# Kernel optimization log

Measured on AMD Instinct MI355X. Metric: run time of the kernel, lower is better.

The kernel has to match this reference:

```python
import jax, jax.numpy as jnp
import numpy as np

BETA = 0.6666666666666666
ZETA = 1.1
GAMMA = -0.1

B, N, D = 256, 128, 64


def setup_inputs() -> dict:
    key = jax.random.key(0)
    kq, kk, kv, km = jax.random.split(key, 4)
    query = jax.random.normal(kq, (B, 1, N, 1, D), dtype=jnp.float32)
    key_t = jax.random.normal(kk, (B, 1, N, 1, D), dtype=jnp.float32)
    value = jax.random.normal(kv, (B, 1, N, 1, D), dtype=jnp.float32)
    # nn.Parameter init: normal(mean=0, std=0.001)
    matrix = jax.random.normal(km, (N, N, D, D), dtype=jnp.float32) * 0.001
    return {"query": query, "key": key_t, "value": value, "matrix": matrix}


def _hard_concrete_gate(log_alpha):
    # deterministic (eval-mode) hard-concrete gate
    s = jax.nn.sigmoid(log_alpha) * (ZETA - GAMMA) + GAMMA
    z = jnp.clip(s, 0.0, 1.0)
    # expected L0 penalty
    l0 = jnp.sum(jax.nn.sigmoid(log_alpha - BETA * np.log(-GAMMA / ZETA)))
    return z, l0


def reference(query, key, value, matrix):
    d = query.shape[-1]
    q = query[:, 0, :, 0, :]   # [B, N, D]
    k = key[:, 0, :, 0, :]     # [B, N, D]
    v = value[:, 0, :, 0, :]   # [B, N, D]
    z, l0 = _hard_concrete_gate(matrix)  # z: [N, N, D, D]
    # score[b,i,j] = sum_{d,e} q[b,i,d] * k[b,j,e] * z[i,j,d,e] / sqrt(D)
    # fused bilinear contraction (no (B,N,N,D,D) intermediate)
    score = jnp.einsum('bid,ijde,bje->bij', q, z, k) / jnp.asarray(
        float(d) ** 0.5, q.dtype)
    attn = jax.nn.softmax(score, axis=-1)          # [B, N, N]
    out = jnp.einsum('bij,bjd->bid', attn, v)      # [B, N, D]
    return out, l0
```

## Files before the change

### kernel.cpp

```cpp
#include <hip/hip_runtime.h>
#include <hip/hip_bf16.h>

#define B_ 256
#define N_ 128
#define D_ 64

typedef short bf16x8 __attribute__((ext_vector_type(8)));
typedef short bf16x4 __attribute__((ext_vector_type(4)));
typedef float f32x4 __attribute__((ext_vector_type(4)));

static __device__ __forceinline__ short f2bf(float f) {
  unsigned u = __builtin_bit_cast(unsigned, f);
  u += 0x7FFFu + ((u >> 16) & 1u);
  return (short)(u >> 16);
}

static __device__ __forceinline__ float sigmoidf_fast(float x) {
  return __builtin_amdgcn_rcpf(1.0f + __expf(-x));
}

__global__ __launch_bounds__(256)
void score_k(const float* __restrict__ qg, const float* __restrict__ kg,
             const float* __restrict__ mat, float* __restrict__ score,
             float* __restrict__ l0g) {
  __shared__ short qs[B_ * 72];
  __shared__ short zs[D_ * 72];

  const int i    = blockIdx.y;
  const int j0   = blockIdx.x * 8;
  const int tid  = threadIdx.x;
  const int w    = tid >> 6;
  const int lane = tid & 63;
  const int quad = lane >> 4;
  const int c    = lane & 15;

  {
    const int d4 = (tid & 15) * 4;
    const int bb = tid >> 4;
    for (int r = 0; r < 16; ++r) {
      const int b = r * 16 + bb;
      const float4 v = *(const float4*)(qg + ((size_t)b * (N_ * D_) + (size_t)i * D_ + d4));
      bf16x4 p;
      p[0] = f2bf(v.x); p[1] = f2bf(v.y); p[2] = f2bf(v.z); p[3] = f2bf(v.w);
      *(bf16x4*)(&qs[b * 72 + d4]) = p;
    }
  }

  float l0p = 0.0f;

  for (int jj = 0; jj < 8; ++jj) {
    const int j = j0 + jj;
    __syncthreads();

    {
      const int d  = tid >> 2;
      const int e0 = (tid & 3) << 4;
      const float4* src = (const float4*)(mat + (((size_t)(i * N_ + j)) << 12) + ((size_t)tid << 4));
      float4 f[4];
      f[0] = src[0]; f[1] = src[1]; f[2] = src[2]; f[3] = src[3];
      const float* fe = (const float*)f;
      #pragma unroll
      for (int u = 0; u < 16; ++u) {
        const float x  = fe[u];
        const float sg = sigmoidf_fast(x);
        const float z  = fminf(fmaxf(sg * 1.2f - 0.1f, 0.0f), 1.0f);
        l0p += sigmoidf_fast(x + 1.5985969f);
        zs[(e0 + u) * 72 + d] = f2bf(z);
      }
    }
    __syncthreads();

    f32x4 acc[4][4];
    #pragma unroll
    for (int et = 0; et < 4; ++et)
      #pragma unroll
      for (int bt = 0; bt < 4; ++bt) acc[et][bt] = (f32x4){0.f, 0.f, 0.f, 0.f};

    #pragma unroll
    for (int ks = 0; ks < 2; ++ks) {
      const int db = ks * 32 + quad * 8;
      bf16x8 af[4];
      #pragma unroll
      for (int et = 0; et < 4; ++et)
        af[et] = *(const bf16x8*)(&zs[(et * 16 + c) * 72 + db]);
      #pragma unroll
      for (int bt = 0; bt < 4; ++bt) {
        const bf16x8 bfr = *(const bf16x8*)(&qs[(w * 64 + bt * 16 + c) * 72 + db]);
        #pragma unroll
        for (int et = 0; et < 4; ++et)
          acc[et][bt] = __builtin_amdgcn_mfma_f32_16x16x32_bf16(af[et], bfr, acc[et][bt], 0, 0, 0);
      }
    }

    #pragma unroll
    for (int bt = 0; bt < 4; ++bt) {
      const int b = w * 64 + bt * 16 + c;
      const float* kp = kg + ((size_t)b * (N_ * D_) + (size_t)j * D_);
      float s = 0.0f;
      #pragma unroll
      for (int et = 0; et < 4; ++et) {
        const float4 kv = *(const float4*)(kp + et * 16 + quad * 4);
        s += acc[et][bt][0] * kv.x + acc[et][bt][1] * kv.y +
             acc[et][bt][2] * kv.z + acc[et][bt][3] * kv.w;
      }
      s += __shfl_xor(s, 16, 64);
      s += __shfl_xor(s, 32, 64);
      if (quad == 0)
        score[(size_t)b * (N_ * N_) + (size_t)i * N_ + j] = s * 0.125f;
    }
  }

  #pragma unroll
  for (int off = 32; off >= 1; off >>= 1) l0p += __shfl_xor(l0p, off, 64);
  if (lane == 0) atomicAdd(l0g, l0p);
}

__global__ __launch_bounds__(256)
void attn_k(const float* __restrict__ score, const float* __restrict__ vg,
            const float* __restrict__ l0g, float* __restrict__ out) {
  __shared__ short ps[4][16 * 136];

  const int b    = blockIdx.y;
  const int half = blockIdx.x;
  const int tid  = threadIdx.x;
  const int w    = tid >> 6;
  const int lane = tid & 63;
  const int quad = lane >> 4;
  const int c    = lane & 15;
  const int i0   = half * 64 + w * 16;

  for (int t = 0; t < 16; ++t) {
    const int i = i0 + t;
    const float* sp = score + (size_t)b * (N_ * N_) + (size_t)i * N_;
    const float s0 = sp[lane], s1 = sp[lane + 64];
    float m = fmaxf(s0, s1);
    #pragma unroll
    for (int off = 32; off >= 1; off >>= 1) m = fmaxf(m, __shfl_xor(m, off, 64));
    const float e0 = __expf(s0 - m), e1 = __expf(s1 - m);
    float l = e0 + e1;
    #pragma unroll
    for (int off = 32; off >= 1; off >>= 1) l += __shfl_xor(l, off, 64);
    const float rl = __builtin_amdgcn_rcpf(l);
    ps[w][t * 136 + lane]      = f2bf(e0 * rl);
    ps[w][t * 136 + lane + 64] = f2bf(e1 * rl);
  }
  __syncthreads();

  f32x4 oacc[4];
  #pragma unroll
  for (int dt = 0; dt < 4; ++dt) oacc[dt] = (f32x4){0.f, 0.f, 0.f, 0.f};

  #pragma unroll
  for (int kt = 0; kt < 4; ++kt) {
    const bf16x8 af = *(const bf16x8*)(&ps[w][c * 136 + kt * 32 + quad * 8]);
    const int jb = kt * 32 + quad * 8;
    #pragma unroll
    for (int dt = 0; dt < 4; ++dt) {
      const float* vp = vg + (size_t)b * (N_ * D_) + (size_t)jb * D_ + dt * 16 + c;
      bf16x8 bfr;
      #pragma unroll
      for (int u = 0; u < 8; ++u) bfr[u] = f2bf(vp[u * D_]);
      oacc[dt] = __builtin_amdgcn_mfma_f32_16x16x32_bf16(af, bfr, oacc[dt], 0, 0, 0);
    }
  }

  #pragma unroll
  for (int dt = 0; dt < 4; ++dt)
    #pragma unroll
    for (int r = 0; r < 4; ++r) {
      const int i = i0 + quad * 4 + r;
      out[(size_t)b * (N_ * D_) + (size_t)i * D_ + dt * 16 + c] = oacc[dt][r];
    }

  if (b == 0 && half == 0 && tid == 0)
    out[(size_t)B_ * N_ * D_] = l0g[0];
}

extern "C" void kernel_launch(void* const* d_in, const int* in_sizes, int n_in,
                              void* d_out, int out_size, void* d_ws, size_t ws_size,
                              hipStream_t stream) {
  const float* q   = (const float*)d_in[0];
  const float* k   = (const float*)d_in[1];
  const float* v   = (const float*)d_in[2];
  const float* mat = (const float*)d_in[3];
  float* out   = (float*)d_out;
  float* score = (float*)d_ws;
  float* l0g   = score + (size_t)B_ * N_ * N_;

  hipMemsetAsync(l0g, 0, sizeof(float), stream);
  score_k<<<dim3(16, 128), 256, 0, stream>>>(q, k, mat, score, l0g);
  attn_k<<<dim3(2, 256), 256, 0, stream>>>(score, v, l0g, out);
}
```

Measured before the change: 560.3 us.

## Prefetch gate matrix in registers, coalesce score writes, stage V in LDS

score_k now handles 16 j columns per block, so the grid shrinks to 8x128, and it prefetches the next j slice of the matrix into registers while the current slice is converted. It also reuses a single exp for both sigmoids, writes scores as float4 vectors per batch row instead of scattered scalars, and uses lighter LDS-only barriers. attn_k loads and transposes V into LDS once per block and prefetches all score rows up front, replacing per-element strided global reads of V. This adds register and LDS pressure, and with fewer blocks occupancy may drop.

```diff
diff --git a/kernel.cpp b/kernel.cpp
--- a/kernel.cpp
+++ b/kernel.cpp
@@ -4,6 +4,7 @@
 #define B_ 256
 #define N_ 128
 #define D_ 64
+#define JT 16
 
 typedef short bf16x8 __attribute__((ext_vector_type(8)));
 typedef short bf16x4 __attribute__((ext_vector_type(4)));
@@ -15,8 +16,8 @@
   return (short)(u >> 16);
 }
 
-static __device__ __forceinline__ float sigmoidf_fast(float x) {
-  return __builtin_amdgcn_rcpf(1.0f + __expf(-x));
+static __device__ __forceinline__ void barrier_lds() {
+  asm volatile("s_waitcnt lgkmcnt(0)\n\ts_barrier" ::: "memory");
 }
 
 __global__ __launch_bounds__(256)
@@ -27,7 +28,7 @@
   __shared__ short zs[D_ * 72];
 
   const int i    = blockIdx.y;
-  const int j0   = blockIdx.x * 8;
+  const int j0   = blockIdx.x * JT;
   const int tid  = threadIdx.x;
   const int w    = tid >> 6;
   const int lane = tid & 63;
@@ -37,6 +38,7 @@
   {
     const int d4 = (tid & 15) * 4;
     const int bb = tid >> 4;
+    #pragma unroll
     for (int r = 0; r < 16; ++r) {
       const int b = r * 16 + bb;
       const float4 v = *(const float4*)(qg + ((size_t)b * (N_ * D_) + (size_t)i * D_ + d4));
@@ -46,67 +48,107 @@
     }
   }
 
+  const int d0 = (tid >> 4) * 4;
+  const int e0 = (tid & 15) * 4;
+
+  float4 F[4];
+  {
+    const float* src = mat + (((size_t)(i * N_ + j0)) << 12);
+    #pragma unroll
+    for (int r = 0; r < 4; ++r)
+      F[r] = *(const float4*)(src + (d0 + r) * 64 + e0);
+  }
+
   float l0p = 0.0f;
 
-  for (int jj = 0; jj < 8; ++jj) {
-    const int j = j0 + jj;
-    __syncthreads();
+  for (int jo = 0; jo < 4; ++jo) {
+    float sacc[4];
+    #pragma unroll
+    for (int ji = 0; ji < 4; ++ji) {
+      const int jj = jo * 4 + ji;
+
+      short zb[4][4];
+      #pragma unroll
+      for (int r = 0; r < 4; ++r) {
+        #pragma unroll
+        for (int u = 0; u < 4; ++u) {
+          const float x  = ((const float*)&F[r])[u];
+          const float t  = __expf(-x);
+          const float sg = __builtin_amdgcn_rcpf(1.0f + t);
+          const float z  = fminf(fmaxf(fmaf(sg, 1.2f, -0.1f), 0.0f), 1.0f);
+          l0p += __builtin_amdgcn_rcpf(fmaf(t, 0.2021805f, 1.0f));
+          zb[r][u] = f2bf(z);
+        }
+      }
+
+      if (jj < JT - 1) {
+        const float* src = mat + (((size_t)(i * N_ + j0 + jj + 1)) << 12);
+        #pragma unroll
+        for (int r = 0; r < 4; ++r)
+          F[r] = *(const float4*)(src + (d0 + r) * 64 + e0);
+      }
+
+      #pragma unroll
+      for (int u = 0; u < 4; ++u) {
+        bf16x4 p;
+        p[0] = zb[0][u]; p[1] = zb[1][u]; p[2] = zb[2][u]; p[3] = zb[3][u];
+        *(bf16x4*)(&zs[(e0 + u) * 72 + d0]) = p;
+      }
+      barrier_lds();
+
+      f32x4 acc[4][4];
+      #pragma unroll
+      for (int et = 0; et < 4; ++et)
+        #pragma unroll
+        for (int bt = 0; bt < 4; ++bt) acc[et][bt] = (f32x4){0.f, 0.f, 0.f, 0.f};
+
+      #pragma unroll
+      for (int ks = 0; ks < 2; ++ks) {
+        const int db = ks * 32 + quad * 8;
+        bf16x8 af[4];
+        #pragma unroll
+        for (int et = 0; et < 4; ++et)
+          af[et] = *(const bf16x8*)(&zs[(et * 16 + c) * 72 + db]);
+        #pragma unroll
+        for (int bt = 0; bt < 4; ++bt) {
+          const bf16x8 bfr = *(const bf16x8*)(&qs[(w * 64 + bt * 16 + c) * 72 + db]);
+          #pragma unroll
+          for (int et = 0; et < 4; ++et)
+            acc[et][bt] = __builtin_amdgcn_mfma_f32_16x16x32_bf16(af[et], bfr, acc[et][bt], 0, 0, 0);
+        }
+      }
+
+      const int j = j0 + jj;
+      float s[4];
+      #pragma unroll
+      for (int bt = 0; bt < 4; ++bt) {
+        const int b = w * 64 + bt * 16 + c;
+        const float* kp = kg + ((size_t)b * (N_ * D_) + (size_t)j * D_);
+        float sv = 0.0f;
+        #pragma unroll
+        for (int et = 0; et < 4; ++et) {
+          const float4 kv = *(const float4*)(kp + et * 16 + quad * 4);
+          sv += acc[et][bt][0] * kv.x + acc[et][bt][1] * kv.y +
+                acc[et][bt][2] * kv.z + acc[et][bt][3] * kv.w;
+        }
+        s[bt] = sv;
+      }
+      barrier_lds();
+
+      #pragma unroll
+      for (int bt = 0; bt < 4; ++bt) {
+        s[bt] += __shfl_xor(s[bt], 16, 64);
+        s[bt] += __shfl_xor(s[bt], 32, 64);
+      }
+      const float sel = quad == 0 ? s[0] : quad == 1 ? s[1] : quad == 2 ? s[2] : s[3];
+      sacc[ji] = sel * 0.125f;
+    }
 
     {
-      const int d  = tid >> 2;
-      const int e0 = (tid & 3) << 4;
-      const float4* src = (const float4*)(mat + (((size_t)(i * N_ + j)) << 12) + ((size_t)tid << 4));
-      float4 f[4];
-      f[0] = src[0]; f[1] = src[1]; f[2] = src[2]; f[3] = src[3];
-      const float* fe = (const float*)f;
-      #pragma unroll
-      for (int u = 0; u < 16; ++u) {
-        const float x  = fe[u];
-        const float sg = sigmoidf_fast(x);
-        const float z  = fminf(fmaxf(sg * 1.2f - 0.1f, 0.0f), 1.0f);
-        l0p += sigmoidf_fast(x + 1.5985969f);
-        zs[(e0 + u) * 72 + d] = f2bf(z);
-      }
-    }
-    __syncthreads();
-
-    f32x4 acc[4][4];
-    #pragma unroll
-    for (int et = 0; et < 4; ++et)
-      #pragma unroll
-      for (int bt = 0; bt < 4; ++bt) acc[et][bt] = (f32x4){0.f, 0.f, 0.f, 0.f};
-
-    #pragma unroll
-    for (int ks = 0; ks < 2; ++ks) {
-      const int db = ks * 32 + quad * 8;
-      bf16x8 af[4];
-      #pragma unroll
-      for (int et = 0; et < 4; ++et)
-        af[et] = *(const bf16x8*)(&zs[(et * 16 + c) * 72 + db]);
-      #pragma unroll
-      for (int bt = 0; bt < 4; ++bt) {
-        const bf16x8 bfr = *(const bf16x8*)(&qs[(w * 64 + bt * 16 + c) * 72 + db]);
-        #pragma unroll
-        for (int et = 0; et < 4; ++et)
-          acc[et][bt] = __builtin_amdgcn_mfma_f32_16x16x32_bf16(af[et], bfr, acc[et][bt], 0, 0, 0);
-      }
-    }
-
-    #pragma unroll
-    for (int bt = 0; bt < 4; ++bt) {
-      const int b = w * 64 + bt * 16 + c;
-      const float* kp = kg + ((size_t)b * (N_ * D_) + (size_t)j * D_);
-      float s = 0.0f;
-      #pragma unroll
-      for (int et = 0; et < 4; ++et) {
-        const float4 kv = *(const float4*)(kp + et * 16 + quad * 4);
-        s += acc[et][bt][0] * kv.x + acc[et][bt][1] * kv.y +
-             acc[et][bt][2] * kv.z + acc[et][bt][3] * kv.w;
-      }
-      s += __shfl_xor(s, 16, 64);
-      s += __shfl_xor(s, 32, 64);
-      if (quad == 0)
-        score[(size_t)b * (N_ * N_) + (size_t)i * N_ + j] = s * 0.125f;
+      const int b_own = w * 64 + lane;
+      f32x4 o;
+      o[0] = sacc[0]; o[1] = sacc[1]; o[2] = sacc[2]; o[3] = sacc[3];
+      *(f32x4*)(score + (size_t)b_own * (N_ * N_) + (size_t)i * N_ + (j0 + jo * 4)) = o;
     }
   }
 
@@ -118,6 +160,7 @@
 __global__ __launch_bounds__(256)
 void attn_k(const float* __restrict__ score, const float* __restrict__ vg,
             const float* __restrict__ l0g, float* __restrict__ out) {
+  __shared__ short vt[D_ * 136];
   __shared__ short ps[4][16 * 136];
 
   const int b    = blockIdx.y;
@@ -129,14 +172,34 @@
   const int c    = lane & 15;
   const int i0   = half * 64 + w * 16;
 
+  {
+    const float* vb = vg + (size_t)b * (N_ * D_);
+    #pragma unroll
+    for (int r = 0; r < 8; ++r) {
+      const int f  = r * 256 + tid;
+      const int j  = f >> 4;
+      const int dd = (f & 15) * 4;
+      const float4 vv = *(const float4*)(vb + j * D_ + dd);
+      vt[(dd + 0) * 136 + j] = f2bf(vv.x);
+      vt[(dd + 1) * 136 + j] = f2bf(vv.y);
+      vt[(dd + 2) * 136 + j] = f2bf(vv.z);
+      vt[(dd + 3) * 136 + j] = f2bf(vv.w);
+    }
+  }
+
+  float s0[16], s1[16];
+  const float* sp0 = score + (size_t)b * (N_ * N_) + (size_t)i0 * N_;
+  #pragma unroll
   for (int t = 0; t < 16; ++t) {
-    const int i = i0 + t;
-    const float* sp = score + (size_t)b * (N_ * N_) + (size_t)i * N_;
-    const float s0 = sp[lane], s1 = sp[lane + 64];
-    float m = fmaxf(s0, s1);
+    s0[t] = sp0[t * N_ + lane];
+    s1[t] = sp0[t * N_ + lane + 64];
+  }
+  #pragma unroll
+  for (int t = 0; t < 16; ++t) {
+    float m = fmaxf(s0[t], s1[t]);
     #pragma unroll
     for (int off = 32; off >= 1; off >>= 1) m = fmaxf(m, __shfl_xor(m, off, 64));
-    const float e0 = __expf(s0 - m), e1 = __expf(s1 - m);
+    const float e0 = __expf(s0[t] - m), e1 = __expf(s1[t] - m);
     float l = e0 + e1;
     #pragma unroll
     for (int off = 32; off >= 1; off >>= 1) l += __shfl_xor(l, off, 64);
@@ -144,7 +207,7 @@
     ps[w][t * 136 + lane]      = f2bf(e0 * rl);
     ps[w][t * 136 + lane + 64] = f2bf(e1 * rl);
   }
-  __syncthreads();
+  barrier_lds();
 
   f32x4 oacc[4];
   #pragma unroll
@@ -152,14 +215,11 @@
 
   #pragma unroll
   for (int kt = 0; kt < 4; ++kt) {
-    const bf16x8 af = *(const bf16x8*)(&ps[w][c * 136 + kt * 32 + quad * 8]);
     const int jb = kt * 32 + quad * 8;
+    const bf16x8 af = *(const bf16x8*)(&ps[w][c * 136 + jb]);
     #pragma unroll
     for (int dt = 0; dt < 4; ++dt) {
-      const float* vp = vg + (size_t)b * (N_ * D_) + (size_t)jb * D_ + dt * 16 + c;
-      bf16x8 bfr;
-      #pragma unroll
-      for (int u = 0; u < 8; ++u) bfr[u] = f2bf(vp[u * D_]);
+      const bf16x8 bfr = *(const bf16x8*)(&vt[(dt * 16 + c) * 136 + jb]);
       oacc[dt] = __builtin_amdgcn_mfma_f32_16x16x32_bf16(af, bfr, oacc[dt], 0, 0, 0);
     }
   }
@@ -188,6 +248,6 @@
   float* l0g   = score + (size_t)B_ * N_ * N_;
 
   hipMemsetAsync(l0g, 0, sizeof(float), stream);
-  score_k<<<dim3(16, 128), 256, 0, stream>>>(q, k, mat, score, l0g);
-  attn_k<<<dim3(2, 256), 256, 0, stream>>>(score, v, l0g, out);
-}
+  score_k<<<dim3(N_ / JT, N_), 256, 0, stream>>>(q, k, mat, score, l0g);
+  attn_k<<<dim3(2, B_), 256, 0, stream>>>(score, v, l0g, out);
+}
```

New measurement: 529.9 us. 1.06x faster.
